# Performance work log

Hardware: AMD Instinct MI355X
Metric: run time of the kernel (lower is better)

## Reference

```python
import jax, jax.numpy as jnp
import numpy as np

N = 100000
E = 1_600_000
IN_DIM = 128
HIDDEN = 128


def spmm(row, col, vals, H):
    # y[r] = sum_{edges e with row[e]==r} vals[e] * H[col[e]]
    msgs = vals[:, None] * H[col]          # [E, hidden] gather + scale
    return jax.ops.segment_sum(msgs, row, num_segments=H.shape[0])


def setup_inputs() -> dict:
    key = jax.random.key(0)
    ks = jax.random.split(key, 10)
    X = jax.random.normal(ks[0], (N, IN_DIM), dtype=jnp.float32)
    row = jax.random.randint(ks[1], (E,), 0, N, dtype=jnp.int32)
    col = jax.random.randint(ks[2], (E,), 0, N, dtype=jnp.int32)
    vals = jax.random.uniform(ks[3], (E,), dtype=jnp.float32)
    s_in = 1.0 / np.sqrt(IN_DIM)
    s_h = 1.0 / np.sqrt(HIDDEN)
    W_in = jax.random.normal(ks[4], (IN_DIM, HIDDEN), dtype=jnp.float32) * s_in
    b_in = jax.random.normal(ks[5], (HIDDEN,), dtype=jnp.float32) * s_in
    W_mp1 = jax.random.normal(ks[6], (HIDDEN, HIDDEN), dtype=jnp.float32) * s_h
    W_mp2 = jax.random.normal(ks[7], (HIDDEN, HIDDEN), dtype=jnp.float32) * s_h
    W_out = jax.random.normal(ks[8], (HIDDEN, 1), dtype=jnp.float32) * s_h
    b_out = jax.random.normal(ks[9], (1,), dtype=jnp.float32) * s_h
    return {"X": X, "row": row, "col": col, "vals": vals,
            "W_in": W_in, "b_in": b_in, "W_mp1": W_mp1, "W_mp2": W_mp2,
            "W_out": W_out, "b_out": b_out}


def reference(X, row, col, vals, W_in, b_in, W_mp1, W_mp2, W_out, b_out):
    H = jax.nn.relu(X @ W_in + b_in)          # [N, hidden]
    AH = spmm(row, col, vals, H)              # 1-hop propagation
    A2H = spmm(row, col, vals, AH)            # 2-hop propagation
    H2 = jax.nn.relu(AH @ W_mp1 + A2H @ W_mp2)
    return H2 @ W_out + b_out                 # [N, 1]
```

## Files before the change

kernel.cpp:

```cpp
#include <hip/hip_runtime.h>

#define N_NODES 100000
#define N_EDGES 1600000
#define NBUCK 391
#define NCHUNK 256
#define CHUNK 6250
#define LROW 136
#define DCAP 5120

typedef float f32x4 __attribute__((ext_vector_type(4)));
typedef _Float16 f16x8 __attribute__((ext_vector_type(8)));
typedef _Float16 h16x2 __attribute__((ext_vector_type(2)));

__device__ __forceinline__ unsigned f2h_bits(float f) {
    union { _Float16 h; unsigned short s; } c;
    c.h = (_Float16)f;
    return c.s;
}
__device__ __forceinline__ h16x2 u2h(unsigned u) {
    union { unsigned u; h16x2 h; } c;
    c.u = u;
    return c.h;
}
__device__ __forceinline__ unsigned pk16lo(unsigned hi, unsigned lo) {
    return __builtin_amdgcn_perm(hi, lo, 0x05040100u);
}
__device__ __forceinline__ unsigned pk16hi(unsigned hi, unsigned lo) {
    return __builtin_amdgcn_perm(hi, lo, 0x07060302u);
}
__device__ __forceinline__ float fdot2(h16x2 a, h16x2 b, float c) {
#if __has_builtin(__builtin_amdgcn_fdot2)
    return __builtin_amdgcn_fdot2(a, b, c, false);
#else
    return c + (float)a[0] * (float)b[0] + (float)a[1] * (float)b[1];
#endif
}

__device__ __forceinline__ f16x8 pack_h8(float4 a, float4 b) {
    f16x8 r;
    r[0] = (_Float16)a.x; r[1] = (_Float16)a.y;
    r[2] = (_Float16)a.z; r[3] = (_Float16)a.w;
    r[4] = (_Float16)b.x; r[5] = (_Float16)b.y;
    r[6] = (_Float16)b.z; r[7] = (_Float16)b.w;
    return r;
}


__global__ __launch_bounds__(256) void k_binA(const int* __restrict__ row,
                                              int* __restrict__ hmat) {
    __shared__ int h[NBUCK];
    for (int i = threadIdx.x; i < NBUCK; i += 256) h[i] = 0;
    __syncthreads();
    int s = blockIdx.x * CHUNK, e = s + CHUNK;
    for (int i = s + threadIdx.x; i < e; i += 256)
        atomicAdd(&h[row[i] >> 8], 1);
    __syncthreads();
    for (int b = threadIdx.x; b < NBUCK; b += 256)
        hmat[blockIdx.x * NBUCK + b] = h[b];
}

__global__ __launch_bounds__(256) void k_colscan(const int* __restrict__ hmat,
                                                 int* __restrict__ bases,
                                                 int* __restrict__ bcnt) {
    __shared__ int s[256];
    int b = blockIdx.x, t = threadIdx.x;
    int v = hmat[t * NBUCK + b];
    s[t] = v;
    __syncthreads();
    for (int off = 1; off < 256; off <<= 1) {
        int x = (t >= off) ? s[t - off] : 0;
        __syncthreads();
        s[t] += x;
        __syncthreads();
    }
    bases[t * NBUCK + b] = s[t] - v;
    if (t == 255) bcnt[b] = s[255];
}

__global__ void k_scanB(const int* __restrict__ bcnt, int* __restrict__ bstart) {
    __shared__ int s[512];
    int t = threadIdx.x;
    int v = (t < NBUCK) ? bcnt[t] : 0;
    s[t] = v;
    __syncthreads();
    for (int off = 1; off < 512; off <<= 1) {
        int x = (t >= off) ? s[t - off] : 0;
        __syncthreads();
        s[t] += x;
        __syncthreads();
    }
    if (t < NBUCK) bstart[t] = s[t] - v;
    if (t == NBUCK) bstart[NBUCK] = N_EDGES;
}

__global__ __launch_bounds__(256) void k_binC(const int* __restrict__ row,
                                              const int* __restrict__ col,
                                              const float* __restrict__ vals,
                                              const int* __restrict__ bstart,
                                              const int* __restrict__ bases,
                                              int2* __restrict__ grouped) {
    __shared__ int cnt[NBUCK];
    for (int i = threadIdx.x; i < NBUCK; i += 256) cnt[i] = 0;
    __syncthreads();
    int s = blockIdx.x * CHUNK, e = s + CHUNK;
    for (int i = s + threadIdx.x; i < e; i += 256) {
        int r = row[i];
        int b = r >> 8;
        int rank = atomicAdd(&cnt[b], 1);
        int pos = bstart[b] + bases[blockIdx.x * NBUCK + b] + rank;
        unsigned hv = f2h_bits(vals[i]);
        grouped[pos] = make_int2(col[i], ((r & 255) << 14) | hv);
    }
}

__global__ __launch_bounds__(256) void k_binD(const int2* __restrict__ grouped,
                                              const int* __restrict__ bstart,
                                              unsigned* __restrict__ evf,
                                              int* __restrict__ row_ptr) {
    __shared__ int h[256], sc[256], cur[256];
    __shared__ int2 ebuf[DCAP];
    int b = blockIdx.x, t = threadIdx.x;
    int s0 = bstart[b], e0 = bstart[b + 1];
    int n = e0 - s0;
    bool inlds = (n <= DCAP);
    h[t] = 0;
    __syncthreads();
    if (inlds) {
        for (int i = t; i < n; i += 256) ebuf[i] = grouped[s0 + i];
        __syncthreads();
        for (int i = t; i < n; i += 256)
            atomicAdd(&h[(ebuf[i].y >> 14) & 255], 1);
    } else {
        for (int i = s0 + t; i < e0; i += 256)
            atomicAdd(&h[(grouped[i].y >> 14) & 255], 1);
    }
    __syncthreads();
    int v = h[t];
    sc[t] = v;
    __syncthreads();
    for (int off = 1; off < 256; off <<= 1) {
        int x = (t >= off) ? sc[t - off] : 0;
        __syncthreads();
        sc[t] += x;
        __syncthreads();
    }
    int excl = sc[t] - v;
    cur[t] = excl;
    int grow = b * 256 + t;
    if (grow <= N_NODES) row_ptr[grow] = s0 + excl;
    __syncthreads();
    if (inlds) {
        for (int i = t; i < n; i += 256) {
            int2 g = ebuf[i];
            int rl = (g.y >> 14) & 255;
            int p = atomicAdd(&cur[rl], 1);
            evf[s0 + p] = ((unsigned)g.x << 14) | (unsigned)(g.y & 0x3fff);
        }
    } else {
        for (int i = s0 + t; i < e0; i += 256) {
            int2 g = grouped[i];
            int rl = (g.y >> 14) & 255;
            int p = atomicAdd(&cur[rl], 1);
            evf[s0 + p] = ((unsigned)g.x << 14) | (unsigned)(g.y & 0x3fff);
        }
    }
}

__global__ void k_cvtw3(const float* __restrict__ Wa, const float* __restrict__ Wb,
                        const float* __restrict__ Wc, unsigned short* __restrict__ Wta,
                        unsigned short* __restrict__ Wtb, unsigned short* __restrict__ Wtc) {
    int t = blockIdx.x * 256 + threadIdx.x;
    int which = t >> 14;
    int i = t & 16383;
    int n = i & 127, k = i >> 7;
    const float* W = which == 0 ? Wa : which == 1 ? Wb : Wc;
    unsigned short* Wt = which == 0 ? Wta : which == 1 ? Wtb : Wtc;
    Wt[n * 128 + k] = (unsigned short)f2h_bits(W[k * 128 + n]);
}

__global__ __launch_bounds__(256) void k_gemm_in(const float* __restrict__ X,
                                                 const unsigned short* __restrict__ Wt,
                                                 const float* __restrict__ b,
                                                 unsigned short* __restrict__ H) {
    __shared__ unsigned short lds[64 * LROW];
    int tid = threadIdx.x;
    int lane = tid & 63, wv = tid >> 6;
    int quad = lane >> 4, c16 = lane & 15;

    f16x8 wf[2][4];
    float bb[2];
#pragma unroll
    for (int nt = 0; nt < 2; nt++) {
        int ng = wv * 2 + nt;
        bb[nt] = b[ng * 16 + c16];
#pragma unroll
        for (int kc = 0; kc < 4; kc++)
            wf[nt][kc] = *(const f16x8*)&Wt[(ng * 16 + c16) * 128 + kc * 32 + quad * 8];
    }

    int tilebase = blockIdx.x * 64;
    const float4* Xg = (const float4*)X;
#pragma unroll
    for (int i = 0; i < 4; i++) {
        int c = tid + i * 256;
        int r = c >> 4, o = c & 15;
        int grow = tilebase + r;
        float4 f0 = make_float4(0.f, 0.f, 0.f, 0.f), f1 = f0;
        if (grow < N_NODES) {
            f0 = Xg[(size_t)grow * 32 + o * 2];
            f1 = Xg[(size_t)grow * 32 + o * 2 + 1];
        }
        *(f16x8*)&lds[r * LROW + o * 8] = pack_h8(f0, f1);
    }
    __syncthreads();

    f32x4 acc[4][2] = {};
#pragma unroll
    for (int t4 = 0; t4 < 4; t4++) {
#pragma unroll
        for (int kc = 0; kc < 4; kc++) {
            f16x8 af = *(const f16x8*)&lds[(t4 * 16 + c16) * LROW + kc * 32 + quad * 8];
#pragma unroll
            for (int nt = 0; nt < 2; nt++)
                acc[t4][nt] = __builtin_amdgcn_mfma_f32_16x16x32_f16(af, wf[nt][kc],
                                                                    acc[t4][nt], 0, 0, 0);
        }
    }
    __syncthreads();

#pragma unroll
    for (int t4 = 0; t4 < 4; t4++)
#pragma unroll
        for (int nt = 0; nt < 2; nt++) {
            int ncol = (wv * 2 + nt) * 16 + c16;
#pragma unroll
            for (int r = 0; r < 4; r++) {
                float v = fmaxf(acc[t4][nt][r] + bb[nt], 0.f);
                lds[(t4 * 16 + quad * 4 + r) * LROW + ncol] = (unsigned short)f2h_bits(v);
            }
        }
    __syncthreads();
#pragma unroll
    for (int i = 0; i < 4; i++) {
        int c = tid + i * 256;
        int r = c >> 4, o = c & 15;
        int grow = tilebase + r;
        if (grow < N_NODES)
            *(uint4*)&H[(size_t)grow * 128 + o * 8] = *(const uint4*)&lds[r * LROW + o * 8];
    }
}

__global__ __launch_bounds__(256) void k_spmm(const int* __restrict__ rp,
                                              const unsigned* __restrict__ evf,
                                              const unsigned* __restrict__ Hin,
                                              unsigned* __restrict__ Ho) {
    int wid = (blockIdx.x * blockDim.x + threadIdx.x) >> 6;
    int lane = threadIdx.x & 63;
    if (wid >= N_NODES) return;
    int q = lane >> 4, l16 = lane & 15;
    int s = __builtin_amdgcn_readfirstlane(rp[wid]);
    int e = __builtin_amdgcn_readfirstlane(rp[wid + 1]);
    float a0 = 0.f, a1 = 0.f, a2 = 0.f, a3 = 0.f;
    float a4 = 0.f, a5 = 0.f, a6 = 0.f, a7 = 0.f;
    int j = s;
    for (; j + 16 <= e; j += 16) {
        unsigned u0 = evf[j + q];
        unsigned u1 = evf[j + 4 + q];
        unsigned u2 = evf[j + 8 + q];
        unsigned u3 = evf[j + 12 + q];
        const uint4 h0 = *(const uint4*)&Hin[(size_t)(u0 >> 14) * 64 + l16 * 4];
        const uint4 h1 = *(const uint4*)&Hin[(size_t)(u1 >> 14) * 64 + l16 * 4];
        const uint4 h2 = *(const uint4*)&Hin[(size_t)(u2 >> 14) * 64 + l16 * 4];
        const uint4 h3 = *(const uint4*)&Hin[(size_t)(u3 >> 14) * 64 + l16 * 4];
        h16x2 v01 = u2h(pk16lo(u1 & 0x3fffu, u0 & 0x3fffu));
        h16x2 v23 = u2h(pk16lo(u3 & 0x3fffu, u2 & 0x3fffu));
        a0 = fdot2(v01, u2h(pk16lo(h1.x, h0.x)), a0);
        a0 = fdot2(v23, u2h(pk16lo(h3.x, h2.x)), a0);
        a1 = fdot2(v01, u2h(pk16hi(h1.x, h0.x)), a1);
        a1 = fdot2(v23, u2h(pk16hi(h3.x, h2.x)), a1);
        a2 = fdot2(v01, u2h(pk16lo(h1.y, h0.y)), a2);
        a2 = fdot2(v23, u2h(pk16lo(h3.y, h2.y)), a2);
        a3 = fdot2(v01, u2h(pk16hi(h1.y, h0.y)), a3);
        a3 = fdot2(v23, u2h(pk16hi(h3.y, h2.y)), a3);
        a4 = fdot2(v01, u2h(pk16lo(h1.z, h0.z)), a4);
        a4 = fdot2(v23, u2h(pk16lo(h3.z, h2.z)), a4);
        a5 = fdot2(v01, u2h(pk16hi(h1.z, h0.z)), a5);
        a5 = fdot2(v23, u2h(pk16hi(h3.z, h2.z)), a5);
        a6 = fdot2(v01, u2h(pk16lo(h1.w, h0.w)), a6);
        a6 = fdot2(v23, u2h(pk16lo(h3.w, h2.w)), a6);
        a7 = fdot2(v01, u2h(pk16hi(h1.w, h0.w)), a7);
        a7 = fdot2(v23, u2h(pk16hi(h3.w, h2.w)), a7);
    }
    if (j < e) {
        int i0 = j + q, i1 = j + 4 + q, i2 = j + 8 + q, i3 = j + 12 + q;
        unsigned u0 = evf[i0 < e ? i0 : e - 1];
        unsigned u1 = evf[i1 < e ? i1 : e - 1];
        unsigned u2 = evf[i2 < e ? i2 : e - 1];
        unsigned u3 = evf[i3 < e ? i3 : e - 1];
        const uint4 h0 = *(const uint4*)&Hin[(size_t)(u0 >> 14) * 64 + l16 * 4];
        const uint4 h1 = *(const uint4*)&Hin[(size_t)(u1 >> 14) * 64 + l16 * 4];
        const uint4 h2 = *(const uint4*)&Hin[(size_t)(u2 >> 14) * 64 + l16 * 4];
        const uint4 h3 = *(const uint4*)&Hin[(size_t)(u3 >> 14) * 64 + l16 * 4];
        unsigned m0 = (i0 < e) ? (u0 & 0x3fffu) : 0u;
        unsigned m1 = (i1 < e) ? (u1 & 0x3fffu) : 0u;
        unsigned m2 = (i2 < e) ? (u2 & 0x3fffu) : 0u;
        unsigned m3 = (i3 < e) ? (u3 & 0x3fffu) : 0u;
        h16x2 v01 = u2h(pk16lo(m1, m0));
        h16x2 v23 = u2h(pk16lo(m3, m2));
        a0 = fdot2(v01, u2h(pk16lo(h1.x, h0.x)), a0);
        a0 = fdot2(v23, u2h(pk16lo(h3.x, h2.x)), a0);
        a1 = fdot2(v01, u2h(pk16hi(h1.x, h0.x)), a1);
        a1 = fdot2(v23, u2h(pk16hi(h3.x, h2.x)), a1);
        a2 = fdot2(v01, u2h(pk16lo(h1.y, h0.y)), a2);
        a2 = fdot2(v23, u2h(pk16lo(h3.y, h2.y)), a2);
        a3 = fdot2(v01, u2h(pk16hi(h1.y, h0.y)), a3);
        a3 = fdot2(v23, u2h(pk16hi(h3.y, h2.y)), a3);
        a4 = fdot2(v01, u2h(pk16lo(h1.z, h0.z)), a4);
        a4 = fdot2(v23, u2h(pk16lo(h3.z, h2.z)), a4);
        a5 = fdot2(v01, u2h(pk16hi(h1.z, h0.z)), a5);
        a5 = fdot2(v23, u2h(pk16hi(h3.z, h2.z)), a5);
        a6 = fdot2(v01, u2h(pk16lo(h1.w, h0.w)), a6);
        a6 = fdot2(v23, u2h(pk16lo(h3.w, h2.w)), a6);
        a7 = fdot2(v01, u2h(pk16hi(h1.w, h0.w)), a7);
        a7 = fdot2(v23, u2h(pk16hi(h3.w, h2.w)), a7);
    }
    a0 += __shfl_xor(a0, 16, 64); a0 += __shfl_xor(a0, 32, 64);
    a1 += __shfl_xor(a1, 16, 64); a1 += __shfl_xor(a1, 32, 64);
    a2 += __shfl_xor(a2, 16, 64); a2 += __shfl_xor(a2, 32, 64);
    a3 += __shfl_xor(a3, 16, 64); a3 += __shfl_xor(a3, 32, 64);
    a4 += __shfl_xor(a4, 16, 64); a4 += __shfl_xor(a4, 32, 64);
    a5 += __shfl_xor(a5, 16, 64); a5 += __shfl_xor(a5, 32, 64);
    a6 += __shfl_xor(a6, 16, 64); a6 += __shfl_xor(a6, 32, 64);
    a7 += __shfl_xor(a7, 16, 64); a7 += __shfl_xor(a7, 32, 64);
    if (q == 0) {
        uint4 p;
        p.x = (f2h_bits(a1) << 16) | f2h_bits(a0);
        p.y = (f2h_bits(a3) << 16) | f2h_bits(a2);
        p.z = (f2h_bits(a5) << 16) | f2h_bits(a4);
        p.w = (f2h_bits(a7) << 16) | f2h_bits(a6);
        *(uint4*)&Ho[(size_t)wid * 64 + l16 * 4] = p;
    }
}

__global__ __launch_bounds__(256) void k_gemm_out(const unsigned short* __restrict__ AH,
                                                  const unsigned short* __restrict__ A2H,
                                                  const unsigned short* __restrict__ Wt1,
                                                  const unsigned short* __restrict__ Wt2,
                                                  const float* __restrict__ Wout,
                                                  const float* __restrict__ bout,
                                                  float* __restrict__ out) {
    __shared__ unsigned short lds[2][64 * LROW];
    __shared__ float part[4][64];
    int tid = threadIdx.x;
    int lane = tid & 63, wv = tid >> 6;
    int quad = lane >> 4, c16 = lane & 15;

    f16x8 w1f[2][4], w2f[2][4];
    float wo[2];
#pragma unroll
    for (int nt = 0; nt < 2; nt++) {
        int ng = wv * 2 + nt;
        wo[nt] = Wout[ng * 16 + c16];
#pragma unroll
        for (int kc = 0; kc < 4; kc++) {
            w1f[nt][kc] = *(const f16x8*)&Wt1[(ng * 16 + c16) * 128 + kc * 32 + quad * 8];
            w2f[nt][kc] = *(const f16x8*)&Wt2[(ng * 16 + c16) * 128 + kc * 32 + quad * 8];
        }
    }
    float bo = bout[0];

    int tilebase = blockIdx.x * 64;
    const uint4* Ag = (const uint4*)(AH + (size_t)tilebase * 128);
    const uint4* Bg = (const uint4*)(A2H + (size_t)tilebase * 128);
#pragma unroll
    for (int i = 0; i < 4; i++) {
        int c = tid + i * 256;
        int r = c >> 4, o = c & 15;
        *(uint4*)&lds[0][r * LROW + o * 8] = Ag[c];
        *(uint4*)&lds[1][r * LROW + o * 8] = Bg[c];
    }
    __syncthreads();

    f32x4 acc[4][2] = {};
#pragma unroll
    for (int t4 = 0; t4 < 4; t4++) {
#pragma unroll
        for (int kc = 0; kc < 4; kc++) {
            f16x8 afA = *(const f16x8*)&lds[0][(t4 * 16 + c16) * LROW + kc * 32 + quad * 8];
            f16x8 afB = *(const f16x8*)&lds[1][(t4 * 16 + c16) * LROW + kc * 32 + quad * 8];
#pragma unroll
            for (int nt = 0; nt < 2; nt++) {
                acc[t4][nt] = __builtin_amdgcn_mfma_f32_16x16x32_f16(afA, w1f[nt][kc],
                                                                    acc[t4][nt], 0, 0, 0);
                acc[t4][nt] = __builtin_amdgcn_mfma_f32_16x16x32_f16(afB, w2f[nt][kc],
                                                                    acc[t4][nt], 0, 0, 0);
            }
        }
    }

#pragma unroll
    for (int t4 = 0; t4 < 4; t4++) {
        float p[4];
#pragma unroll
        for (int r = 0; r < 4; r++)
            p[r] = fmaxf(acc[t4][0][r], 0.f) * wo[0] + fmaxf(acc[t4][1][r], 0.f) * wo[1];
#pragma unroll
        for (int m = 1; m < 16; m <<= 1)
#pragma unroll
            for (int r = 0; r < 4; r++) p[r] += __shfl_xor(p[r], m, 64);
        if (c16 == 0)
#pragma unroll
            for (int r = 0; r < 4; r++) part[wv][t4 * 16 + quad * 4 + r] = p[r];
    }
    __syncthreads();
    if (tid < 64) {
        int orow = tilebase + tid;
        if (orow < N_NODES)
            out[orow] = part[0][tid] + part[1][tid] + part[2][tid] + part[3][tid] + bo;
    }
}


extern "C" void kernel_launch(void* const* d_in, const int* in_sizes, int n_in,
                              void* d_out, int out_size, void* d_ws, size_t ws_size,
                              hipStream_t stream) {
    const float* X    = (const float*)d_in[0];
    const int*   row  = (const int*)d_in[1];
    const int*   col  = (const int*)d_in[2];
    const float* vals = (const float*)d_in[3];
    const float* W_in = (const float*)d_in[4];
    const float* b_in = (const float*)d_in[5];
    const float* W1   = (const float*)d_in[6];
    const float* W2   = (const float*)d_in[7];
    const float* Wout = (const float*)d_in[8];
    const float* bout = (const float*)d_in[9];
    float* out = (float*)d_out;

    char* ws = (char*)d_ws;
    size_t off = 0;
    auto alloc = [&](size_t bytes) -> void* {
        void* p = ws + off;
        off += (bytes + 511) & ~(size_t)511;
        return p;
    };
    unsigned short* Hb  = (unsigned short*)alloc((size_t)N_NODES * 128 * 2);
    unsigned short* AHb = (unsigned short*)alloc((size_t)N_NODES * 128 * 2);
    unsigned short* A2b = (unsigned short*)alloc((size_t)N_NODES * 128 * 2);
    unsigned* evf  = (unsigned*)alloc((size_t)N_EDGES * 4);
    int2* grouped  = (int2*)alloc((size_t)N_EDGES * 8);
    unsigned short* Wtin = (unsigned short*)alloc(128 * 128 * 2);
    unsigned short* Wt1  = (unsigned short*)alloc(128 * 128 * 2);
    unsigned short* Wt2  = (unsigned short*)alloc(128 * 128 * 2);
    int*   hmat    = (int*)alloc((size_t)NCHUNK * NBUCK * 4);
    int*   bases   = (int*)alloc((size_t)NCHUNK * NBUCK * 4);
    int*   bcnt    = (int*)alloc(512 * 4);
    int*   bstart  = (int*)alloc(512 * 4);
    int*   row_ptr = (int*)alloc((size_t)(N_NODES + 256) * 4);

    k_binA<<<NCHUNK, 256, 0, stream>>>(row, hmat);
    k_colscan<<<NBUCK, 256, 0, stream>>>(hmat, bases, bcnt);
    k_scanB<<<1, 512, 0, stream>>>(bcnt, bstart);
    k_binC<<<NCHUNK, 256, 0, stream>>>(row, col, vals, bstart, bases, grouped);
    k_binD<<<NBUCK, 256, 0, stream>>>(grouped, bstart, evf, row_ptr);

    k_cvtw3<<<192, 256, 0, stream>>>(W_in, W1, W2, Wtin, Wt1, Wt2);

    int gblk = (N_NODES + 63) / 64;
    k_gemm_in<<<gblk, 256, 0, stream>>>(X, Wtin, b_in, Hb);

    int sblk = (N_NODES + 3) / 4;
    k_spmm<<<sblk, 256, 0, stream>>>(row_ptr, evf, (const unsigned*)Hb, (unsigned*)AHb);
    k_spmm<<<sblk, 256, 0, stream>>>(row_ptr, evf, (const unsigned*)AHb, (unsigned*)A2b);

    k_gemm_out<<<gblk, 256, 0, stream>>>(AHb, A2b, Wt1, Wt2, Wout, bout, out);
}
```

Baseline: 317.8 us.

## Merge preprocessing kernels and load edge lists once per wavefront via shuffles

Folds the weight transpose/convert kernel into the histogram kernel and merges the per-bucket column scan with the bucket-total scan, which removes two kernel launches and their serialization gaps. The second merged kernel has one extra block that recomputes bucket totals serially across all chunks. The SpMM kernel now loads up to 64 packed edge words with one coalesced load per wavefront and distributes them with shuffles, replacing the four redundant per-quarter loads of each edge. This adds shuffle instructions and an outer loop in exchange.

```diff
diff --git a/kernel.cpp b/kernel.cpp
--- a/kernel.cpp
+++ b/kernel.cpp
@@ -46,51 +46,67 @@
 }
 
 
-__global__ __launch_bounds__(256) void k_binA(const int* __restrict__ row,
-                                              int* __restrict__ hmat) {
-    __shared__ int h[NBUCK];
-    for (int i = threadIdx.x; i < NBUCK; i += 256) h[i] = 0;
-    __syncthreads();
-    int s = blockIdx.x * CHUNK, e = s + CHUNK;
-    for (int i = s + threadIdx.x; i < e; i += 256)
-        atomicAdd(&h[row[i] >> 8], 1);
-    __syncthreads();
-    for (int b = threadIdx.x; b < NBUCK; b += 256)
-        hmat[blockIdx.x * NBUCK + b] = h[b];
-}
-
-__global__ __launch_bounds__(256) void k_colscan(const int* __restrict__ hmat,
-                                                 int* __restrict__ bases,
-                                                 int* __restrict__ bcnt) {
-    __shared__ int s[256];
+__global__ __launch_bounds__(256) void k_prep(const int* __restrict__ row,
+                                              int* __restrict__ hmat,
+                                              const float* __restrict__ Wa,
+                                              const float* __restrict__ Wb,
+                                              const float* __restrict__ Wc,
+                                              unsigned short* __restrict__ Wta,
+                                              unsigned short* __restrict__ Wtb,
+                                              unsigned short* __restrict__ Wtc) {
+    if (blockIdx.x < NCHUNK) {
+        __shared__ int h[NBUCK];
+        for (int i = threadIdx.x; i < NBUCK; i += 256) h[i] = 0;
+        __syncthreads();
+        int s = blockIdx.x * CHUNK, e = s + CHUNK;
+        for (int i = s + threadIdx.x; i < e; i += 256)
+            atomicAdd(&h[row[i] >> 8], 1);
+        __syncthreads();
+        for (int b = threadIdx.x; b < NBUCK; b += 256)
+            hmat[blockIdx.x * NBUCK + b] = h[b];
+    } else {
+        int t = (blockIdx.x - NCHUNK) * 256 + threadIdx.x;
+        int which = t >> 14;
+        int i = t & 16383;
+        int n = i & 127, k = i >> 7;
+        const float* W = which == 0 ? Wa : which == 1 ? Wb : Wc;
+        unsigned short* Wt = which == 0 ? Wta : which == 1 ? Wtb : Wtc;
+        Wt[n * 128 + k] = (unsigned short)f2h_bits(W[k * 128 + n]);
+    }
+}
+
+__global__ __launch_bounds__(512) void k_colscanB(const int* __restrict__ hmat,
+                                                  int* __restrict__ bases,
+                                                  int* __restrict__ bstart) {
+    __shared__ int s[512];
     int b = blockIdx.x, t = threadIdx.x;
-    int v = hmat[t * NBUCK + b];
-    s[t] = v;
-    __syncthreads();
-    for (int off = 1; off < 256; off <<= 1) {
-        int x = (t >= off) ? s[t - off] : 0;
-        __syncthreads();
-        s[t] += x;
-        __syncthreads();
-    }
-    bases[t * NBUCK + b] = s[t] - v;
-    if (t == 255) bcnt[b] = s[255];
-}
-
-__global__ void k_scanB(const int* __restrict__ bcnt, int* __restrict__ bstart) {
-    __shared__ int s[512];
-    int t = threadIdx.x;
-    int v = (t < NBUCK) ? bcnt[t] : 0;
-    s[t] = v;
-    __syncthreads();
-    for (int off = 1; off < 512; off <<= 1) {
-        int x = (t >= off) ? s[t - off] : 0;
-        __syncthreads();
-        s[t] += x;
-        __syncthreads();
-    }
-    if (t < NBUCK) bstart[t] = s[t] - v;
-    if (t == NBUCK) bstart[NBUCK] = N_EDGES;
+    if (b < NBUCK) {
+        int v = (t < NCHUNK) ? hmat[t * NBUCK + b] : 0;
+        s[t] = v;
+        __syncthreads();
+        for (int off = 1; off < 512; off <<= 1) {
+            int x = (t >= off) ? s[t - off] : 0;
+            __syncthreads();
+            s[t] += x;
+            __syncthreads();
+        }
+        if (t < NCHUNK) bases[t * NBUCK + b] = s[t] - v;
+    } else {
+        int v = 0;
+        if (t < NBUCK) {
+            for (int blk = 0; blk < NCHUNK; blk++) v += hmat[blk * NBUCK + t];
+        }
+        s[t] = v;
+        __syncthreads();
+        for (int off = 1; off < 512; off <<= 1) {
+            int x = (t >= off) ? s[t - off] : 0;
+            __syncthreads();
+            s[t] += x;
+            __syncthreads();
+        }
+        if (t < NBUCK) bstart[t] = s[t] - v;
+        if (t == NBUCK) bstart[NBUCK] = N_EDGES;
+    }
 }
 
 __global__ __launch_bounds__(256) void k_binC(const int* __restrict__ row,
@@ -164,18 +180,6 @@
             evf[s0 + p] = ((unsigned)g.x << 14) | (unsigned)(g.y & 0x3fff);
         }
     }
-}
-
-__global__ void k_cvtw3(const float* __restrict__ Wa, const float* __restrict__ Wb,
-                        const float* __restrict__ Wc, unsigned short* __restrict__ Wta,
-                        unsigned short* __restrict__ Wtb, unsigned short* __restrict__ Wtc) {
-    int t = blockIdx.x * 256 + threadIdx.x;
-    int which = t >> 14;
-    int i = t & 16383;
-    int n = i & 127, k = i >> 7;
-    const float* W = which == 0 ? Wa : which == 1 ? Wb : Wc;
-    unsigned short* Wt = which == 0 ? Wta : which == 1 ? Wtb : Wtc;
-    Wt[n * 128 + k] = (unsigned short)f2h_bits(W[k * 128 + n]);
 }
 
 __global__ __launch_bounds__(256) void k_gemm_in(const float* __restrict__ X,
@@ -262,67 +266,72 @@
     int e = __builtin_amdgcn_readfirstlane(rp[wid + 1]);
     float a0 = 0.f, a1 = 0.f, a2 = 0.f, a3 = 0.f;
     float a4 = 0.f, a5 = 0.f, a6 = 0.f, a7 = 0.f;
-    int j = s;
-    for (; j + 16 <= e; j += 16) {
-        unsigned u0 = evf[j + q];
-        unsigned u1 = evf[j + 4 + q];
-        unsigned u2 = evf[j + 8 + q];
-        unsigned u3 = evf[j + 12 + q];
-        const uint4 h0 = *(const uint4*)&Hin[(size_t)(u0 >> 14) * 64 + l16 * 4];
-        const uint4 h1 = *(const uint4*)&Hin[(size_t)(u1 >> 14) * 64 + l16 * 4];
-        const uint4 h2 = *(const uint4*)&Hin[(size_t)(u2 >> 14) * 64 + l16 * 4];
-        const uint4 h3 = *(const uint4*)&Hin[(size_t)(u3 >> 14) * 64 + l16 * 4];
-        h16x2 v01 = u2h(pk16lo(u1 & 0x3fffu, u0 & 0x3fffu));
-        h16x2 v23 = u2h(pk16lo(u3 & 0x3fffu, u2 & 0x3fffu));
-        a0 = fdot2(v01, u2h(pk16lo(h1.x, h0.x)), a0);
-        a0 = fdot2(v23, u2h(pk16lo(h3.x, h2.x)), a0);
-        a1 = fdot2(v01, u2h(pk16hi(h1.x, h0.x)), a1);
-        a1 = fdot2(v23, u2h(pk16hi(h3.x, h2.x)), a1);
-        a2 = fdot2(v01, u2h(pk16lo(h1.y, h0.y)), a2);
-        a2 = fdot2(v23, u2h(pk16lo(h3.y, h2.y)), a2);
-        a3 = fdot2(v01, u2h(pk16hi(h1.y, h0.y)), a3);
-        a3 = fdot2(v23, u2h(pk16hi(h3.y, h2.y)), a3);
-        a4 = fdot2(v01, u2h(pk16lo(h1.z, h0.z)), a4);
-        a4 = fdot2(v23, u2h(pk16lo(h3.z, h2.z)), a4);
-        a5 = fdot2(v01, u2h(pk16hi(h1.z, h0.z)), a5);
-        a5 = fdot2(v23, u2h(pk16hi(h3.z, h2.z)), a5);
-        a6 = fdot2(v01, u2h(pk16lo(h1.w, h0.w)), a6);
-        a6 = fdot2(v23, u2h(pk16lo(h3.w, h2.w)), a6);
-        a7 = fdot2(v01, u2h(pk16hi(h1.w, h0.w)), a7);
-        a7 = fdot2(v23, u2h(pk16hi(h3.w, h2.w)), a7);
-    }
-    if (j < e) {
-        int i0 = j + q, i1 = j + 4 + q, i2 = j + 8 + q, i3 = j + 12 + q;
-        unsigned u0 = evf[i0 < e ? i0 : e - 1];
-        unsigned u1 = evf[i1 < e ? i1 : e - 1];
-        unsigned u2 = evf[i2 < e ? i2 : e - 1];
-        unsigned u3 = evf[i3 < e ? i3 : e - 1];
-        const uint4 h0 = *(const uint4*)&Hin[(size_t)(u0 >> 14) * 64 + l16 * 4];
-        const uint4 h1 = *(const uint4*)&Hin[(size_t)(u1 >> 14) * 64 + l16 * 4];
-        const uint4 h2 = *(const uint4*)&Hin[(size_t)(u2 >> 14) * 64 + l16 * 4];
-        const uint4 h3 = *(const uint4*)&Hin[(size_t)(u3 >> 14) * 64 + l16 * 4];
-        unsigned m0 = (i0 < e) ? (u0 & 0x3fffu) : 0u;
-        unsigned m1 = (i1 < e) ? (u1 & 0x3fffu) : 0u;
-        unsigned m2 = (i2 < e) ? (u2 & 0x3fffu) : 0u;
-        unsigned m3 = (i3 < e) ? (u3 & 0x3fffu) : 0u;
-        h16x2 v01 = u2h(pk16lo(m1, m0));
-        h16x2 v23 = u2h(pk16lo(m3, m2));
-        a0 = fdot2(v01, u2h(pk16lo(h1.x, h0.x)), a0);
-        a0 = fdot2(v23, u2h(pk16lo(h3.x, h2.x)), a0);
-        a1 = fdot2(v01, u2h(pk16hi(h1.x, h0.x)), a1);
-        a1 = fdot2(v23, u2h(pk16hi(h3.x, h2.x)), a1);
-        a2 = fdot2(v01, u2h(pk16lo(h1.y, h0.y)), a2);
-        a2 = fdot2(v23, u2h(pk16lo(h3.y, h2.y)), a2);
-        a3 = fdot2(v01, u2h(pk16hi(h1.y, h0.y)), a3);
-        a3 = fdot2(v23, u2h(pk16hi(h3.y, h2.y)), a3);
-        a4 = fdot2(v01, u2h(pk16lo(h1.z, h0.z)), a4);
-        a4 = fdot2(v23, u2h(pk16lo(h3.z, h2.z)), a4);
-        a5 = fdot2(v01, u2h(pk16hi(h1.z, h0.z)), a5);
-        a5 = fdot2(v23, u2h(pk16hi(h3.z, h2.z)), a5);
-        a6 = fdot2(v01, u2h(pk16lo(h1.w, h0.w)), a6);
-        a6 = fdot2(v23, u2h(pk16lo(h3.w, h2.w)), a6);
-        a7 = fdot2(v01, u2h(pk16hi(h1.w, h0.w)), a7);
-        a7 = fdot2(v23, u2h(pk16hi(h3.w, h2.w)), a7);
+    for (int base = s; base < e; base += 64) {
+        int cnt = e - base;
+        if (cnt > 64) cnt = 64;
+        unsigned ev = evf[base + (lane < cnt ? lane : cnt - 1)];
+        int r = 0;
+        for (; r + 16 <= cnt; r += 16) {
+            unsigned u0 = __shfl(ev, r + q, 64);
+            unsigned u1 = __shfl(ev, r + 4 + q, 64);
+            unsigned u2 = __shfl(ev, r + 8 + q, 64);
+            unsigned u3 = __shfl(ev, r + 12 + q, 64);
+            const uint4 h0 = *(const uint4*)&Hin[(size_t)(u0 >> 14) * 64 + l16 * 4];
+            const uint4 h1 = *(const uint4*)&Hin[(size_t)(u1 >> 14) * 64 + l16 * 4];
+            const uint4 h2 = *(const uint4*)&Hin[(size_t)(u2 >> 14) * 64 + l16 * 4];
+            const uint4 h3 = *(const uint4*)&Hin[(size_t)(u3 >> 14) * 64 + l16 * 4];
+            h16x2 v01 = u2h(pk16lo(u1 & 0x3fffu, u0 & 0x3fffu));
+            h16x2 v23 = u2h(pk16lo(u3 & 0x3fffu, u2 & 0x3fffu));
+            a0 = fdot2(v01, u2h(pk16lo(h1.x, h0.x)), a0);
+            a0 = fdot2(v23, u2h(pk16lo(h3.x, h2.x)), a0);
+            a1 = fdot2(v01, u2h(pk16hi(h1.x, h0.x)), a1);
+            a1 = fdot2(v23, u2h(pk16hi(h3.x, h2.x)), a1);
+            a2 = fdot2(v01, u2h(pk16lo(h1.y, h0.y)), a2);
+            a2 = fdot2(v23, u2h(pk16lo(h3.y, h2.y)), a2);
+            a3 = fdot2(v01, u2h(pk16hi(h1.y, h0.y)), a3);
+            a3 = fdot2(v23, u2h(pk16hi(h3.y, h2.y)), a3);
+            a4 = fdot2(v01, u2h(pk16lo(h1.z, h0.z)), a4);
+            a4 = fdot2(v23, u2h(pk16lo(h3.z, h2.z)), a4);
+            a5 = fdot2(v01, u2h(pk16hi(h1.z, h0.z)), a5);
+            a5 = fdot2(v23, u2h(pk16hi(h3.z, h2.z)), a5);
+            a6 = fdot2(v01, u2h(pk16lo(h1.w, h0.w)), a6);
+            a6 = fdot2(v23, u2h(pk16lo(h3.w, h2.w)), a6);
+            a7 = fdot2(v01, u2h(pk16hi(h1.w, h0.w)), a7);
+            a7 = fdot2(v23, u2h(pk16hi(h3.w, h2.w)), a7);
+        }
+        if (r < cnt) {
+            int i0 = r + q, i1 = r + 4 + q, i2 = r + 8 + q, i3 = r + 12 + q;
+            unsigned u0 = __shfl(ev, i0 < cnt ? i0 : cnt - 1, 64);
+            unsigned u1 = __shfl(ev, i1 < cnt ? i1 : cnt - 1, 64);
+            unsigned u2 = __shfl(ev, i2 < cnt ? i2 : cnt - 1, 64);
+            unsigned u3 = __shfl(ev, i3 < cnt ? i3 : cnt - 1, 64);
+            const uint4 h0 = *(const uint4*)&Hin[(size_t)(u0 >> 14) * 64 + l16 * 4];
+            const uint4 h1 = *(const uint4*)&Hin[(size_t)(u1 >> 14) * 64 + l16 * 4];
+            const uint4 h2 = *(const uint4*)&Hin[(size_t)(u2 >> 14) * 64 + l16 * 4];
+            const uint4 h3 = *(const uint4*)&Hin[(size_t)(u3 >> 14) * 64 + l16 * 4];
+            unsigned m0 = (i0 < cnt) ? (u0 & 0x3fffu) : 0u;
+            unsigned m1 = (i1 < cnt) ? (u1 & 0x3fffu) : 0u;
+            unsigned m2 = (i2 < cnt) ? (u2 & 0x3fffu) : 0u;
+            unsigned m3 = (i3 < cnt) ? (u3 & 0x3fffu) : 0u;
+            h16x2 v01 = u2h(pk16lo(m1, m0));
+            h16x2 v23 = u2h(pk16lo(m3, m2));
+            a0 = fdot2(v01, u2h(pk16lo(h1.x, h0.x)), a0);
+            a0 = fdot2(v23, u2h(pk16lo(h3.x, h2.x)), a0);
+            a1 = fdot2(v01, u2h(pk16hi(h1.x, h0.x)), a1);
+            a1 = fdot2(v23, u2h(pk16hi(h3.x, h2.x)), a1);
+            a2 = fdot2(v01, u2h(pk16lo(h1.y, h0.y)), a2);
+            a2 = fdot2(v23, u2h(pk16lo(h3.y, h2.y)), a2);
+            a3 = fdot2(v01, u2h(pk16hi(h1.y, h0.y)), a3);
+            a3 = fdot2(v23, u2h(pk16hi(h3.y, h2.y)), a3);
+            a4 = fdot2(v01, u2h(pk16lo(h1.z, h0.z)), a4);
+            a4 = fdot2(v23, u2h(pk16lo(h3.z, h2.z)), a4);
+            a5 = fdot2(v01, u2h(pk16hi(h1.z, h0.z)), a5);
+            a5 = fdot2(v23, u2h(pk16hi(h3.z, h2.z)), a5);
+            a6 = fdot2(v01, u2h(pk16lo(h1.w, h0.w)), a6);
+            a6 = fdot2(v23, u2h(pk16lo(h3.w, h2.w)), a6);
+            a7 = fdot2(v01, u2h(pk16hi(h1.w, h0.w)), a7);
+            a7 = fdot2(v23, u2h(pk16hi(h3.w, h2.w)), a7);
+        }
     }
     a0 += __shfl_xor(a0, 16, 64); a0 += __shfl_xor(a0, 32, 64);
     a1 += __shfl_xor(a1, 16, 64); a1 += __shfl_xor(a1, 32, 64);
@@ -453,17 +462,13 @@
     unsigned short* Wt2  = (unsigned short*)alloc(128 * 128 * 2);
     int*   hmat    = (int*)alloc((size_t)NCHUNK * NBUCK * 4);
     int*   bases   = (int*)alloc((size_t)NCHUNK * NBUCK * 4);
-    int*   bcnt    = (int*)alloc(512 * 4);
     int*   bstart  = (int*)alloc(512 * 4);
     int*   row_ptr = (int*)alloc((size_t)(N_NODES + 256) * 4);
 
-    k_binA<<<NCHUNK, 256, 0, stream>>>(row, hmat);
-    k_colscan<<<NBUCK, 256, 0, stream>>>(hmat, bases, bcnt);
-    k_scanB<<<1, 512, 0, stream>>>(bcnt, bstart);
+    k_prep<<<NCHUNK + 192, 256, 0, stream>>>(row, hmat, W_in, W1, W2, Wtin, Wt1, Wt2);
+    k_colscanB<<<NBUCK + 1, 512, 0, stream>>>(hmat, bases, bstart);
     k_binC<<<NCHUNK, 256, 0, stream>>>(row, col, vals, bstart, bases, grouped);
     k_binD<<<NBUCK, 256, 0, stream>>>(grouped, bstart, evf, row_ptr);
-
-    k_cvtw3<<<192, 256, 0, stream>>>(W_in, W1, W2, Wtin, Wt1, Wt2);
 
     int gblk = (N_NODES + 63) / 64;
     k_gemm_in<<<gblk, 256, 0, stream>>>(X, Wtin, b_in, Hb);
```

Result: faster. 296.5 us (-6.7%).
